# Kernel optimization log

Measured on AMD Instinct MI355X. Metric: run time of the kernel, lower is better.

## Reference

```python
import jax, jax.numpy as jnp
import numpy as np

B, L, DIM, H = 1, 2048, 1536, 24
HD = DIM // H  # head_dim = 64
EPS = 1e-6


def _rmsnorm(x, g):
    # RMSNorm over last dim with learnable scale (matches RMSNorm with elementwise_affine=True)
    return x * jax.lax.rsqrt(jnp.mean(x * x, axis=-1, keepdims=True) + EPS) * g


def setup_inputs() -> dict:
    key = jax.random.key(0)
    ks = jax.random.split(key, 4)
    s = 0.02
    return {
        "x": jax.random.normal(ks[0], (B, L, DIM), jnp.float32),
        "w_qkv": jax.random.normal(ks[1], (3 * DIM, DIM), jnp.float32) * s,
        "b_qkv": jnp.zeros((3 * DIM,), jnp.float32),
        "w_proj": jax.random.normal(ks[2], (DIM, DIM), jnp.float32) * s,
        "b_proj": jnp.zeros((DIM,), jnp.float32),
        "g_q": jnp.ones((HD,), jnp.float32),
        "g_k": jnp.ones((HD,), jnp.float32),
    }


def reference(x, w_qkv, b_qkv, w_proj, b_proj, g_q, g_k):
    Bb, Ll, C = x.shape
    # fused QKV projection: [B,L,C] -> [B,L,3C] -> [B,L,3,H,HD]
    qkv = (x @ w_qkv.T + b_qkv).reshape(Bb, Ll, 3, H, HD)
    q, k, v = qkv[:, :, 0], qkv[:, :, 1], qkv[:, :, 2]  # each [B,L,H,HD]
    # per-head RMS norm on q/k (qk_norm='rms')
    q = _rmsnorm(q, g_q)
    k = _rmsnorm(k, g_k)
    # scaled dot-product attention (torch SDPA default scale = 1/sqrt(head_dim))
    scale = 1.0 / np.sqrt(HD).astype(np.float32)
    scores = jnp.einsum('bqhd,bkhd->bhqk', q, k) * scale  # [B,H,L,L]
    attn = jax.nn.softmax(scores, axis=-1)
    o = jnp.einsum('bhqk,bkhd->bqhd', attn, v).reshape(Bb, Ll, C)
    # output projection
    return o @ w_proj.T + b_proj
```

## Files before the change

kernel.cpp:

```cpp
#include <hip/hip_runtime.h>
#include <stdint.h>

#define L_SEQ 2048
#define DIM 1536
#define NH 24
#define HD 64
#define NQKV 4608

typedef unsigned short u16;
typedef __attribute__((ext_vector_type(4))) float f32x4;
typedef __attribute__((ext_vector_type(8))) short bf16x8;
typedef __attribute__((ext_vector_type(4))) u16 u16x4;
typedef __attribute__((ext_vector_type(8))) u16 u16x8;

__device__ __forceinline__ u16 f2bf(float f) {
  unsigned u = __builtin_bit_cast(unsigned, f);
  u += 0x7fffu + ((u >> 16) & 1u);
  return (u16)(u >> 16);
}
__device__ __forceinline__ float b2f(u16 u) {
  return __builtin_bit_cast(float, (unsigned)u << 16);
}

__device__ __forceinline__ void gload_lds16(const void* g, void* lds) {
  __builtin_amdgcn_global_load_lds(
      (const __attribute__((address_space(1))) unsigned int*)g,
      (__attribute__((address_space(3))) unsigned int*)lds, 16, 0, 0);
}

__global__ __launch_bounds__(256) void cast_kernel(const float* __restrict__ in,
                                                   u16* __restrict__ out, int n4) {
  int i = blockIdx.x * 256 + threadIdx.x;
  if (i >= n4) return;
  f32x4 v = ((const f32x4*)in)[i];
  u16x4 o;
  o.x = f2bf(v.x);
  o.y = f2bf(v.y);
  o.z = f2bf(v.z);
  o.w = f2bf(v.w);
  ((u16x4*)out)[i] = o;
}

template <int WRITE_BF16>
__global__ __launch_bounds__(256) void gemm_bt(const u16* __restrict__ A,
                                               const u16* __restrict__ B,
                                               const float* __restrict__ bias,
                                               void* __restrict__ Cout,
                                               int M, int N, int K) {
  __shared__ u16 As[128 * 32];
  __shared__ u16 Bs[128 * 32];
  const int nb = N >> 7;
  const int bx = (int)blockIdx.x % nb;
  const int by = (int)blockIdx.x / nb;
  const int tid = threadIdx.x;
  const int lane = tid & 63;
  const int wv = tid >> 6;
  const int wr = wv >> 1, wc = wv & 1;

  f32x4 acc[4][4];
#pragma unroll
  for (int i = 0; i < 4; i++)
#pragma unroll
    for (int j = 0; j < 4; j++) acc[i][j] = (f32x4)(0.0f);

  const int e0 = tid * 8;
  const int r0 = e0 >> 5, c0 = e0 & 31;
  const u16* Ag0 = A + (size_t)(by * 128 + r0) * K + c0;
  const u16* Ag1 = A + (size_t)(by * 128 + r0 + 64) * K + c0;
  const u16* Bg0 = B + (size_t)(bx * 128 + r0) * K + c0;
  const u16* Bg1 = B + (size_t)(bx * 128 + r0 + 64) * K + c0;
  char* AsB = (char*)As + wv * 1024;
  char* BsB = (char*)Bs + wv * 1024;
  const int kc = (lane >> 4) * 8;

  for (int k0 = 0; k0 < K; k0 += 32) {
    __syncthreads();
    gload_lds16(Ag0 + k0, AsB);
    gload_lds16(Ag1 + k0, AsB + 4096);
    gload_lds16(Bg0 + k0, BsB);
    gload_lds16(Bg1 + k0, BsB + 4096);
    __syncthreads();

    bf16x8 af[4], bfr[4];
#pragma unroll
    for (int mt = 0; mt < 4; mt++)
      af[mt] = *(const bf16x8*)&As[(wr * 64 + mt * 16 + (lane & 15)) * 32 + kc];
#pragma unroll
    for (int nt = 0; nt < 4; nt++)
      bfr[nt] = *(const bf16x8*)&Bs[(wc * 64 + nt * 16 + (lane & 15)) * 32 + kc];
#pragma unroll
    for (int mt = 0; mt < 4; mt++)
#pragma unroll
      for (int nt = 0; nt < 4; nt++)
        acc[mt][nt] = __builtin_amdgcn_mfma_f32_16x16x32_bf16(af[mt], bfr[nt],
                                                              acc[mt][nt], 0, 0, 0);
  }

  const int colb = bx * 128 + wc * 64 + (lane & 15);
  const int rowb = by * 128 + wr * 64 + ((lane >> 4) << 2);
#pragma unroll
  for (int nt = 0; nt < 4; nt++) {
    const int col = colb + nt * 16;
    const float bv = bias[col];
#pragma unroll
    for (int mt = 0; mt < 4; mt++) {
#pragma unroll
      for (int r = 0; r < 4; r++) {
        const int row = rowb + mt * 16 + r;
        float v = acc[mt][nt][r] + bv;
        if (WRITE_BF16)
          ((u16*)Cout)[(size_t)row * N + col] = f2bf(v);
        else
          ((float*)Cout)[(size_t)row * N + col] = v;
      }
    }
  }
}

__global__ __launch_bounds__(256) void qkvnorm_kernel(const u16* __restrict__ qkv,
                                                      const float* __restrict__ gq,
                                                      const float* __restrict__ gk,
                                                      u16* __restrict__ Qh,
                                                      u16* __restrict__ Kh,
                                                      u16* __restrict__ Vt) {
  const int h = blockIdx.y;
  const int lblk = blockIdx.x * 64;
  const int tid = threadIdx.x;
  const int lane = tid & 63, wv = tid >> 6;
  __shared__ u16 vt[64][64];
  const float gqv = gq[lane] * 0.125f * 1.44269504088896f;
  const float gkv = gk[lane];
#pragma unroll 1
  for (int i = 0; i < 16; i++) {
    const int l = lblk + wv * 16 + i;
    const size_t base = (size_t)l * NQKV + h * HD + lane;
    const float q = b2f(qkv[base]);
    const float k = b2f(qkv[base + DIM]);
    float sq = q * q, sk = k * k;
#pragma unroll
    for (int m = 32; m; m >>= 1) {
      sq += __shfl_xor(sq, m);
      sk += __shfl_xor(sk, m);
    }
    const float rq = rsqrtf(sq * (1.0f / 64.0f) + 1e-6f);
    const float rk = rsqrtf(sk * (1.0f / 64.0f) + 1e-6f);
    const size_t ho = ((size_t)h * L_SEQ + l) * HD + lane;
    Qh[ho] = f2bf(q * rq * gqv);
    Kh[ho] = f2bf(k * rk * gkv);
    vt[wv * 16 + i][lane] = qkv[base + 2 * DIM];
  }
  __syncthreads();
  const int d = tid >> 2;
  const int cb = (tid & 3) * 16;
  u16* dst = Vt + ((size_t)h * HD + d) * L_SEQ + lblk + cb;
#pragma unroll
  for (int j0 = 0; j0 < 4; j0++) {
    u16x4 o;
    o.x = vt[cb + j0 * 4 + 0][d];
    o.y = vt[cb + j0 * 4 + 1][d];
    o.z = vt[cb + j0 * 4 + 2][d];
    o.w = vt[cb + j0 * 4 + 3][d];
    *(u16x4*)(dst + j0 * 4) = o;
  }
}

__global__ __launch_bounds__(256) void flash_kernel(const u16* __restrict__ Qh,
                                                    const u16* __restrict__ Kh,
                                                    const u16* __restrict__ Vt,
                                                    u16* __restrict__ O) {
  const int h = blockIdx.y;
  const int qblk = blockIdx.x * 64;
  const int tid = threadIdx.x;
  const int lane = tid & 63, wv = tid >> 6;
  __shared__ u16 Ks[64][64];
  __shared__ u16 Vs[64][64];
  __shared__ u16 Ps[4][16][64];

  const int l4 = lane & 15;
  const int kc = (lane >> 4) * 8;
  const int swz = (lane & 7) << 3;

  const int qrow = qblk + wv * 16 + l4;
  const u16* Qp = Qh + ((size_t)h * L_SEQ + qrow) * HD;
  const bf16x8 qf0 = *(const bf16x8*)(Qp + kc);
  const bf16x8 qf1 = *(const bf16x8*)(Qp + 32 + kc);
  const bf16x8 ones = (bf16x8)(short)0x3F80;

  f32x4 oacc[4];
#pragma unroll
  for (int dt = 0; dt < 4; dt++) oacc[dt] = (f32x4)(0.0f);
  float mr = -1e30f;
  float lr[4] = {0.f, 0.f, 0.f, 0.f};

  const int krow = tid >> 3;
  const int kcol = (tid & 7) * 8;
  const u16* Kg = Kh + (size_t)h * L_SEQ * HD + (size_t)krow * HD + kcol;
  u16* KsW0 = &Ks[krow][kcol ^ ((krow & 7) << 3)];
  u16* KsW1 = KsW0 + 32 * 64;
  const int vd = tid >> 2;
  const int vcol = (tid & 3) * 16;
  const u16* Vg = Vt + ((size_t)h * HD + vd) * L_SEQ;
  u16* VsW0 = &Vs[vd][vcol ^ ((vd & 7) << 3)];
  u16* VsW1 = &Vs[vd][(vcol + 8) ^ ((vd & 7) << 3)];

  bf16x8 kr0 = *(const bf16x8*)(Kg);
  bf16x8 kr1 = *(const bf16x8*)(Kg + 32 * HD);
  bf16x8 vr0 = *(const bf16x8*)(Vg + vcol);
  bf16x8 vr1 = *(const bf16x8*)(Vg + vcol + 8);

  for (int kb = 0; kb < L_SEQ; kb += 64) {
    __syncthreads();
    *(bf16x8*)KsW0 = kr0;
    *(bf16x8*)KsW1 = kr1;
    *(bf16x8*)VsW0 = vr0;
    *(bf16x8*)VsW1 = vr1;
    if (kb + 64 < L_SEQ) {
      kr0 = *(const bf16x8*)(Kg + (size_t)(kb + 64) * HD);
      kr1 = *(const bf16x8*)(Kg + (size_t)(kb + 96) * HD);
      vr0 = *(const bf16x8*)(Vg + kb + 64 + vcol);
      vr1 = *(const bf16x8*)(Vg + kb + 72 + vcol);
    }
    __syncthreads();

    f32x4 s[4];
    __builtin_amdgcn_s_setprio(1);
#pragma unroll
    for (int st = 0; st < 4; st++) {
      const u16* kp = &Ks[st * 16 + l4][0];
      bf16x8 ka = *(const bf16x8*)(kp + (kc ^ swz));
      bf16x8 kb2 = *(const bf16x8*)(kp + ((kc + 32) ^ swz));
      s[st] = __builtin_amdgcn_mfma_f32_16x16x32_bf16(qf0, ka, (f32x4)(0.0f), 0, 0, 0);
      s[st] = __builtin_amdgcn_mfma_f32_16x16x32_bf16(qf1, kb2, s[st], 0, 0, 0);
    }
    __builtin_amdgcn_s_setprio(0);

    float mx;
    {
      float a0 = fmaxf(fmaxf(s[0][0], s[0][1]), fmaxf(s[0][2], s[0][3]));
      float a1 = fmaxf(fmaxf(s[1][0], s[1][1]), fmaxf(s[1][2], s[1][3]));
      float a2 = fmaxf(fmaxf(s[2][0], s[2][1]), fmaxf(s[2][2], s[2][3]));
      float a3 = fmaxf(fmaxf(s[3][0], s[3][1]), fmaxf(s[3][2], s[3][3]));
      mx = fmaxf(fmaxf(a0, a1), fmaxf(a2, a3));
      mx = fmaxf(mx, __shfl_xor(mx, 1));
      mx = fmaxf(mx, __shfl_xor(mx, 2));
      mx = fmaxf(mx, __shfl_xor(mx, 4));
      mx = fmaxf(mx, __shfl_xor(mx, 8));
      mx = fmaxf(mx, __shfl_xor(mx, 16));
      mx = fmaxf(mx, __shfl_xor(mx, 32));
    }
    if (mx > mr) {
      const float scl = __builtin_amdgcn_exp2f(mr - mx);
      mr = mx;
#pragma unroll
      for (int r = 0; r < 4; r++) lr[r] *= scl;
#pragma unroll
      for (int dt = 0; dt < 4; dt++)
#pragma unroll
        for (int r = 0; r < 4; r++) oacc[dt][r] *= scl;
    }

#pragma unroll
    for (int r = 0; r < 4; r++) {
      const int qr = (lane >> 4) * 4 + r;
      const int wsw = (qr & 7) << 3;
      u16* pr = &Ps[wv][qr][0];
      pr[l4 ^ wsw] = f2bf(__builtin_amdgcn_exp2f(s[0][r] - mr));
      pr[(16 + l4) ^ wsw] = f2bf(__builtin_amdgcn_exp2f(s[1][r] - mr));
      pr[(32 + l4) ^ wsw] = f2bf(__builtin_amdgcn_exp2f(s[2][r] - mr));
      pr[(48 + l4) ^ wsw] = f2bf(__builtin_amdgcn_exp2f(s[3][r] - mr));
    }

    const u16* pp = &Ps[wv][l4][0];
    bf16x8 pf0 = *(const bf16x8*)(pp + (kc ^ swz));
    bf16x8 pf1 = *(const bf16x8*)(pp + ((kc + 32) ^ swz));
    __builtin_amdgcn_s_setprio(1);
    f32x4 ls = __builtin_amdgcn_mfma_f32_16x16x32_bf16(pf0, ones, (f32x4)(0.0f), 0, 0, 0);
    ls = __builtin_amdgcn_mfma_f32_16x16x32_bf16(pf1, ones, ls, 0, 0, 0);
#pragma unroll
    for (int dt = 0; dt < 4; dt++) {
      const u16* vp = &Vs[dt * 16 + l4][0];
      bf16x8 vf0 = *(const bf16x8*)(vp + (kc ^ swz));
      bf16x8 vf1 = *(const bf16x8*)(vp + ((kc + 32) ^ swz));
      oacc[dt] = __builtin_amdgcn_mfma_f32_16x16x32_bf16(pf0, vf0, oacc[dt], 0, 0, 0);
      oacc[dt] = __builtin_amdgcn_mfma_f32_16x16x32_bf16(pf1, vf1, oacc[dt], 0, 0, 0);
    }
    __builtin_amdgcn_s_setprio(0);
#pragma unroll
    for (int r = 0; r < 4; r++) lr[r] += ls[r];
  }

#pragma unroll
  for (int r = 0; r < 4; r++) {
    const float inv = 1.0f / lr[r];
    const int row = qblk + wv * 16 + (lane >> 4) * 4 + r;
#pragma unroll
    for (int dt = 0; dt < 4; dt++) {
      const int col = h * HD + dt * 16 + l4;
      O[(size_t)row * DIM + col] = f2bf(oacc[dt][r] * inv);
    }
  }
}

extern "C" void kernel_launch(void* const* d_in, const int* in_sizes, int n_in,
                              void* d_out, int out_size, void* d_ws, size_t ws_size,
                              hipStream_t stream) {
  const float* x = (const float*)d_in[0];
  const float* w_qkv = (const float*)d_in[1];
  const float* b_qkv = (const float*)d_in[2];
  const float* w_proj = (const float*)d_in[3];
  const float* b_proj = (const float*)d_in[4];
  const float* g_q = (const float*)d_in[5];
  const float* g_k = (const float*)d_in[6];

  char* ws = (char*)d_ws;
  u16* x_b = (u16*)(ws + 0);
  u16* wqkv_b = (u16*)(ws + 6291456);
  u16* wpj_b = (u16*)(ws + 20447232);
  u16* qkv = (u16*)(ws + 25165824);
  u16* Qh = (u16*)(ws + 44040192);
  u16* Kh = (u16*)(ws + 50331648);
  u16* Vt = (u16*)(ws + 56623104);
  u16* Ob = (u16*)(ws + 62914560);

  cast_kernel<<<(L_SEQ * DIM / 4 + 255) / 256, 256, 0, stream>>>(x, x_b, L_SEQ * DIM / 4);
  cast_kernel<<<(NQKV * DIM / 4 + 255) / 256, 256, 0, stream>>>(w_qkv, wqkv_b, NQKV * DIM / 4);
  cast_kernel<<<(DIM * DIM / 4 + 255) / 256, 256, 0, stream>>>(w_proj, wpj_b, DIM * DIM / 4);

  gemm_bt<1><<<(L_SEQ / 128) * (NQKV / 128), 256, 0, stream>>>(
      x_b, wqkv_b, b_qkv, (void*)qkv, L_SEQ, NQKV, DIM);

  qkvnorm_kernel<<<dim3(L_SEQ / 64, NH), 256, 0, stream>>>(qkv, g_q, g_k, Qh, Kh, Vt);

  flash_kernel<<<dim3(L_SEQ / 64, NH), 256, 0, stream>>>(Qh, Kh, Vt, Ob);

  gemm_bt<0><<<(L_SEQ / 128) * (DIM / 128), 256, 0, stream>>>(
      Ob, wpj_b, b_proj, d_out, L_SEQ, DIM, DIM);
}
```

Measured before the change: 179.1 us.

## Fuse cast kernels, double-buffer GEMM LDS, and transpose flash score layout

Merges the three fp32-to-bf16 cast launches into one grid-stride kernel writing a contiguous workspace. The GEMM gets a double-buffered LDS that prefetches the next K-tile while computing the current one, leaving one barrier per iteration. Flash attention computes S transposed (K as the A operand), so each lane's row max needs only two cross-lane shuffles and P is written to LDS as 4-wide vectors. Rescaling is skipped unless some row's max grows by more than 8 (log2 units). That lazy rescale lets exp2 arguments reach about 2^8, a small numerical risk in bf16 P.

```diff
diff --git a/kernel.cpp b/kernel.cpp
--- a/kernel.cpp
+++ b/kernel.cpp
@@ -28,17 +28,35 @@
       (__attribute__((address_space(3))) unsigned int*)lds, 16, 0, 0);
 }
 
-__global__ __launch_bounds__(256) void cast_kernel(const float* __restrict__ in,
-                                                   u16* __restrict__ out, int n4) {
-  int i = blockIdx.x * 256 + threadIdx.x;
-  if (i >= n4) return;
-  f32x4 v = ((const f32x4*)in)[i];
-  u16x4 o;
-  o.x = f2bf(v.x);
-  o.y = f2bf(v.y);
-  o.z = f2bf(v.z);
-  o.w = f2bf(v.w);
-  ((u16x4*)out)[i] = o;
+__global__ __launch_bounds__(256) void cast3_kernel(const float* __restrict__ x,
+                                                    const float* __restrict__ wq,
+                                                    const float* __restrict__ wp,
+                                                    u16* __restrict__ out) {
+  const int n1 = (L_SEQ * DIM) / 4;
+  const int n2 = (NQKV * DIM) / 4;
+  const int n3 = (DIM * DIM) / 4;
+  const int tot = n1 + n2 + n3;
+  for (int i = blockIdx.x * 256 + threadIdx.x; i < tot; i += gridDim.x * 256) {
+    const f32x4* src;
+    int j;
+    if (i < n1) {
+      src = (const f32x4*)x;
+      j = i;
+    } else if (i < n1 + n2) {
+      src = (const f32x4*)wq;
+      j = i - n1;
+    } else {
+      src = (const f32x4*)wp;
+      j = i - n1 - n2;
+    }
+    f32x4 v = src[j];
+    u16x4 o;
+    o.x = f2bf(v.x);
+    o.y = f2bf(v.y);
+    o.z = f2bf(v.z);
+    o.w = f2bf(v.w);
+    ((u16x4*)out)[i] = o;
+  }
 }
 
 template <int WRITE_BF16>
@@ -47,8 +65,8 @@
                                                const float* __restrict__ bias,
                                                void* __restrict__ Cout,
                                                int M, int N, int K) {
-  __shared__ u16 As[128 * 32];
-  __shared__ u16 Bs[128 * 32];
+  __shared__ u16 As[2][128 * 32];
+  __shared__ u16 Bs[2][128 * 32];
   const int nb = N >> 7;
   const int bx = (int)blockIdx.x % nb;
   const int by = (int)blockIdx.x / nb;
@@ -69,31 +87,41 @@
   const u16* Ag1 = A + (size_t)(by * 128 + r0 + 64) * K + c0;
   const u16* Bg0 = B + (size_t)(bx * 128 + r0) * K + c0;
   const u16* Bg1 = B + (size_t)(bx * 128 + r0 + 64) * K + c0;
-  char* AsB = (char*)As + wv * 1024;
-  char* BsB = (char*)Bs + wv * 1024;
   const int kc = (lane >> 4) * 8;
-
+  const int wb = wv * 1024;
+
+  gload_lds16(Ag0, (char*)As[0] + wb);
+  gload_lds16(Ag1, (char*)As[0] + wb + 4096);
+  gload_lds16(Bg0, (char*)Bs[0] + wb);
+  gload_lds16(Bg1, (char*)Bs[0] + wb + 4096);
+  __syncthreads();
+
+  int cur = 0;
   for (int k0 = 0; k0 < K; k0 += 32) {
-    __syncthreads();
-    gload_lds16(Ag0 + k0, AsB);
-    gload_lds16(Ag1 + k0, AsB + 4096);
-    gload_lds16(Bg0 + k0, BsB);
-    gload_lds16(Bg1 + k0, BsB + 4096);
-    __syncthreads();
-
+    const int nxt = cur ^ 1;
+    if (k0 + 32 < K) {
+      gload_lds16(Ag0 + k0 + 32, (char*)As[nxt] + wb);
+      gload_lds16(Ag1 + k0 + 32, (char*)As[nxt] + wb + 4096);
+      gload_lds16(Bg0 + k0 + 32, (char*)Bs[nxt] + wb);
+      gload_lds16(Bg1 + k0 + 32, (char*)Bs[nxt] + wb + 4096);
+    }
+    const u16* Asc = As[cur];
+    const u16* Bsc = Bs[cur];
     bf16x8 af[4], bfr[4];
 #pragma unroll
     for (int mt = 0; mt < 4; mt++)
-      af[mt] = *(const bf16x8*)&As[(wr * 64 + mt * 16 + (lane & 15)) * 32 + kc];
+      af[mt] = *(const bf16x8*)&Asc[(wr * 64 + mt * 16 + (lane & 15)) * 32 + kc];
 #pragma unroll
     for (int nt = 0; nt < 4; nt++)
-      bfr[nt] = *(const bf16x8*)&Bs[(wc * 64 + nt * 16 + (lane & 15)) * 32 + kc];
+      bfr[nt] = *(const bf16x8*)&Bsc[(wc * 64 + nt * 16 + (lane & 15)) * 32 + kc];
 #pragma unroll
     for (int mt = 0; mt < 4; mt++)
 #pragma unroll
       for (int nt = 0; nt < 4; nt++)
         acc[mt][nt] = __builtin_amdgcn_mfma_f32_16x16x32_bf16(af[mt], bfr[nt],
                                                               acc[mt][nt], 0, 0, 0);
+    __syncthreads();
+    cur = nxt;
   }
 
   const int colb = bx * 128 + wc * 64 + (lane & 15);
@@ -177,8 +205,9 @@
   __shared__ u16 Ps[4][16][64];
 
   const int l4 = lane & 15;
-  const int kc = (lane >> 4) * 8;
-  const int swz = (lane & 7) << 3;
+  const int g = lane >> 4;
+  const int kc = g * 8;
+  const int swz = (l4 & 7) << 3;
 
   const int qrow = qblk + wv * 16 + l4;
   const u16* Qp = Qh + ((size_t)h * L_SEQ + qrow) * HD;
@@ -229,8 +258,8 @@
       const u16* kp = &Ks[st * 16 + l4][0];
       bf16x8 ka = *(const bf16x8*)(kp + (kc ^ swz));
       bf16x8 kb2 = *(const bf16x8*)(kp + ((kc + 32) ^ swz));
-      s[st] = __builtin_amdgcn_mfma_f32_16x16x32_bf16(qf0, ka, (f32x4)(0.0f), 0, 0, 0);
-      s[st] = __builtin_amdgcn_mfma_f32_16x16x32_bf16(qf1, kb2, s[st], 0, 0, 0);
+      s[st] = __builtin_amdgcn_mfma_f32_16x16x32_bf16(ka, qf0, (f32x4)(0.0f), 0, 0, 0);
+      s[st] = __builtin_amdgcn_mfma_f32_16x16x32_bf16(kb2, qf1, s[st], 0, 0, 0);
     }
     __builtin_amdgcn_s_setprio(0);
 
@@ -241,33 +270,33 @@
       float a2 = fmaxf(fmaxf(s[2][0], s[2][1]), fmaxf(s[2][2], s[2][3]));
       float a3 = fmaxf(fmaxf(s[3][0], s[3][1]), fmaxf(s[3][2], s[3][3]));
       mx = fmaxf(fmaxf(a0, a1), fmaxf(a2, a3));
-      mx = fmaxf(mx, __shfl_xor(mx, 1));
-      mx = fmaxf(mx, __shfl_xor(mx, 2));
-      mx = fmaxf(mx, __shfl_xor(mx, 4));
-      mx = fmaxf(mx, __shfl_xor(mx, 8));
       mx = fmaxf(mx, __shfl_xor(mx, 16));
       mx = fmaxf(mx, __shfl_xor(mx, 32));
     }
-    if (mx > mr) {
-      const float scl = __builtin_amdgcn_exp2f(mr - mx);
-      mr = mx;
-#pragma unroll
-      for (int r = 0; r < 4; r++) lr[r] *= scl;
+    if (__any(mx > mr + 8.0f)) {
+      const float nm = fmaxf(mr, mx);
+      const float sclo = __builtin_amdgcn_exp2f(mr - nm);
+      mr = nm;
+      float scl[4];
+#pragma unroll
+      for (int r = 0; r < 4; r++) scl[r] = __shfl(sclo, g * 4 + r);
+#pragma unroll
+      for (int r = 0; r < 4; r++) lr[r] *= scl[r];
 #pragma unroll
       for (int dt = 0; dt < 4; dt++)
 #pragma unroll
-        for (int r = 0; r < 4; r++) oacc[dt][r] *= scl;
-    }
-
-#pragma unroll
-    for (int r = 0; r < 4; r++) {
-      const int qr = (lane >> 4) * 4 + r;
-      const int wsw = (qr & 7) << 3;
-      u16* pr = &Ps[wv][qr][0];
-      pr[l4 ^ wsw] = f2bf(__builtin_amdgcn_exp2f(s[0][r] - mr));
-      pr[(16 + l4) ^ wsw] = f2bf(__builtin_amdgcn_exp2f(s[1][r] - mr));
-      pr[(32 + l4) ^ wsw] = f2bf(__builtin_amdgcn_exp2f(s[2][r] - mr));
-      pr[(48 + l4) ^ wsw] = f2bf(__builtin_amdgcn_exp2f(s[3][r] - mr));
+        for (int r = 0; r < 4; r++) oacc[dt][r] *= scl[r];
+    }
+
+    u16* pr = &Ps[wv][l4][0];
+#pragma unroll
+    for (int st = 0; st < 4; st++) {
+      u16x4 pw;
+      pw.x = f2bf(__builtin_amdgcn_exp2f(s[st][0] - mr));
+      pw.y = f2bf(__builtin_amdgcn_exp2f(s[st][1] - mr));
+      pw.z = f2bf(__builtin_amdgcn_exp2f(s[st][2] - mr));
+      pw.w = f2bf(__builtin_amdgcn_exp2f(s[st][3] - mr));
+      *(u16x4*)(pr + ((st * 16 + g * 4) ^ swz)) = pw;
     }
 
     const u16* pp = &Ps[wv][l4][0];
@@ -292,7 +321,7 @@
 #pragma unroll
   for (int r = 0; r < 4; r++) {
     const float inv = 1.0f / lr[r];
-    const int row = qblk + wv * 16 + (lane >> 4) * 4 + r;
+    const int row = qblk + wv * 16 + g * 4 + r;
 #pragma unroll
     for (int dt = 0; dt < 4; dt++) {
       const int col = h * HD + dt * 16 + l4;
@@ -322,9 +351,7 @@
   u16* Vt = (u16*)(ws + 56623104);
   u16* Ob = (u16*)(ws + 62914560);
 
-  cast_kernel<<<(L_SEQ * DIM / 4 + 255) / 256, 256, 0, stream>>>(x, x_b, L_SEQ * DIM / 4);
-  cast_kernel<<<(NQKV * DIM / 4 + 255) / 256, 256, 0, stream>>>(w_qkv, wqkv_b, NQKV * DIM / 4);
-  cast_kernel<<<(DIM * DIM / 4 + 255) / 256, 256, 0, stream>>>(w_proj, wpj_b, DIM * DIM / 4);
+  cast3_kernel<<<3072, 256, 0, stream>>>(x, w_qkv, w_proj, x_b);
 
   gemm_bt<1><<<(L_SEQ / 128) * (NQKV / 128), 256, 0, stream>>>(
       x_b, wqkv_b, b_qkv, (void*)qkv, L_SEQ, NQKV, DIM);
```

Result: faster. 157.7 us (-12.0%).
